# Performance work log

Hardware: AMD Instinct MI355X
Metric: run time of the kernel (lower is better)

Reference implementation:

```python
import jax, jax.numpy as jnp
import numpy as np

SHARPNESS = 2


def setup_inputs() -> dict:
    key = jax.random.key(0)
    k1, k2, k3 = jax.random.split(key, 3)
    x = jax.random.normal(k1, (16, 256, 48, 48), dtype=jnp.float32)
    # 1x1 conv == per-pixel linear: weight (out_c, in_c), bias (out_c,)
    W = jax.random.normal(k2, (256, 256), dtype=jnp.float32) * 0.0625
    bias = jax.random.normal(k3, (256,), dtype=jnp.float32) * 0.01
    return {"x": x, "W": W, "bias": bias}


def reference(x, W, bias):
    b, c, h, w = x.shape
    hw = h * w
    # sample-wide L2 norm over the full (c*h*w) vector (faithful to source)
    xn = jnp.linalg.norm(x.reshape(b, -1), axis=1).reshape(b, 1, 1)
    # NOTE: raw reshapes of the (b,c,h,w)-contiguous tensor, NOT transposes
    x1 = x.reshape(b, hw, c) / xn
    x2 = x.reshape(b, c, hw) / xn
    cos = jnp.einsum('bnc,bcm->bnm', x1, x2)          # (b, hw, hw)
    s = jnp.maximum(cos, 0.0) ** SHARPNESS            # relu^sharpness
    # transform block: 1x1 conv
    tr = jnp.einsum('oc,bchw->bohw', W, x) + bias[None, :, None, None]
    tr = tr.reshape(b, hw, c)                         # raw reshape, as in source
    y = jnp.einsum('bnm,bmc->bnc', s, tr)             # (b, hw, c)
    return y.reshape(b, c, h, w)
```

## Files before the change

kernel.cpp:

```cpp
#include <hip/hip_runtime.h>

#define NB 16
#define NC 256
#define HW 2304
#define CHW 589824

typedef __attribute__((ext_vector_type(8))) short bf16x8;
typedef __attribute__((ext_vector_type(16))) float f32x16;

union BF8 { bf16x8 v; unsigned short u[8]; unsigned d[4]; };

__device__ inline unsigned short f2bf(float f) {
  unsigned u = __builtin_bit_cast(unsigned, f);
  u += 0x7fffu + ((u >> 16) & 1u);
  return (unsigned short)(u >> 16);
}

__device__ inline unsigned f2bf2(float lo, float hi) {
  unsigned r;
  asm("v_cvt_pk_bf16_f32 %0, %1, %2" : "=v"(r) : "v"(lo), "v"(hi));
  return r;
}

__global__ __launch_bounds__(256) void prep_kernel(const float* __restrict__ x,
                                                   const float* __restrict__ W,
                                                   unsigned short* __restrict__ wp,
                                                   unsigned short* __restrict__ x1p,
                                                   unsigned short* __restrict__ xtp,
                                                   double* __restrict__ partials) {
  __shared__ __align__(16) char smem[33344];
  const int bid = blockIdx.x;
  const int tid = threadIdx.x;

  if (bid < 8) {
    const int rt = bid;
    float* tile = (float*)smem;
    const float4* src = (const float4*)(W + (size_t)rt * 32 * 256);
    #pragma unroll
    for (int it = 0; it < 8; ++it) {
      const int i = tid + 256 * it;
      float4 v = src[i];
      const int fi = 4 * i, row = fi >> 8, col = fi & 255;
      *(float4*)&tile[row * 260 + col] = v;
    }
    __syncthreads();
    const int w = tid >> 6, l = tid & 63, l31 = l & 31, h = l >> 5;
    unsigned short* dst = wp + (size_t)rt * 8192;
    #pragma unroll
    for (int ff = 0; ff < 4; ++ff) {
      const int f = 4 * w + ff;
      const float* rp = &tile[l31 * 260 + 16 * f + 8 * h];
      const float4 r0 = *(const float4*)rp;
      const float4 r1 = *(const float4*)(rp + 4);
      BF8 o;
      o.d[0] = f2bf2(r0.x, r0.y);
      o.d[1] = f2bf2(r0.z, r0.w);
      o.d[2] = f2bf2(r1.x, r1.y);
      o.d[3] = f2bf2(r1.z, r1.w);
      *(bf16x8*)(dst + (((size_t)f) * 64 + l) * 8) = o.v;
    }
  } else if (bid < 8 + 1152) {
    const int e = bid - 8;
    const int nb = e % 72, b = e / 72;
    float* tile = (float*)smem;
    double* red = (double*)(smem + 33280);
    const float4* src = (const float4*)(x + (size_t)b * CHW + nb * 8192);
    double ss = 0.0;
    #pragma unroll
    for (int it = 0; it < 8; ++it) {
      const int i = tid + 256 * it;
      float4 v = src[i];
      const int fi = 4 * i, row = fi >> 8, col = fi & 255;
      *(float4*)&tile[row * 260 + col] = v;
      ss += (double)v.x * v.x + (double)v.y * v.y + (double)v.z * v.z + (double)v.w * v.w;
    }
    #pragma unroll
    for (int off = 32; off > 0; off >>= 1) ss += __shfl_down(ss, off, 64);
    const int w = tid >> 6, l = tid & 63;
    if (l == 0) red[w] = ss;
    __syncthreads();
    if (tid == 0) partials[b * 72 + nb] = red[0] + red[1] + red[2] + red[3];
    const int l31 = l & 31, h = l >> 5;
    unsigned short* dst = x1p + (size_t)b * CHW + (size_t)nb * 8192;
    #pragma unroll
    for (int ff = 0; ff < 4; ++ff) {
      const int f = 4 * w + ff;
      const float* rp = &tile[l31 * 260 + 16 * f + 8 * h];
      const float4 r0 = *(const float4*)rp;
      const float4 r1 = *(const float4*)(rp + 4);
      BF8 o;
      o.d[0] = f2bf2(r0.x, r0.y);
      o.d[1] = f2bf2(r0.z, r0.w);
      o.d[2] = f2bf2(r1.x, r1.y);
      o.d[3] = f2bf2(r1.z, r1.w);
      *(bf16x8*)(dst + (((size_t)f) * 64 + l) * 8) = o.v;
    }
  } else {
    const int e = bid - 1160;
    const int mt = e % 36, kt = (e / 36) % 4, b = e / 144;
    const int m0 = mt * 64, k0 = kt * 64;
    float* tile = (float*)smem;
    const float* xb = x + (size_t)b * CHW;
    #pragma unroll
    for (int it = 0; it < 4; ++it) {
      const int i = tid + 256 * it;
      const int row = i >> 4, c4 = (i & 15) * 4;
      float4 v = *(const float4*)(xb + (size_t)(k0 + row) * HW + m0 + c4);
      *(float4*)&tile[row * 68 + c4] = v;
    }
    __syncthreads();
    const int w = tid >> 6, l = tid & 63, l31 = l & 31, h = l >> 5;
    unsigned short* dst = xtp + (size_t)b * CHW;
    #pragma unroll
    for (int pp = 0; pp < 2; ++pp) {
      const int p = 2 * w + pp, mbl = p >> 2, fl = p & 3;
      BF8 o;
      #pragma unroll
      for (int jj = 0; jj < 4; ++jj) {
        const float e0 = tile[(16 * fl + 8 * h + 2 * jj) * 68 + 32 * mbl + l31];
        const float e1 = tile[(16 * fl + 8 * h + 2 * jj + 1) * 68 + 32 * mbl + l31];
        o.d[jj] = f2bf2(e0, e1);
      }
      const int mb = 2 * mt + mbl, f = 4 * kt + fl;
      *(bf16x8*)(dst + (((size_t)mb * 16 + f) * 64 + l) * 8) = o.v;
    }
  }
}

__global__ __launch_bounds__(512, 1) void conv2_kernel(const unsigned short* __restrict__ wp,
                                                       const float* __restrict__ bias,
                                                       const unsigned short* __restrict__ xtp,
                                                       unsigned short* __restrict__ trp,
                                                       const double* __restrict__ partials,
                                                       float* __restrict__ inv_xn2) {
  const int bid = blockIdx.x;
  if (bid == 128) {
    const int t = threadIdx.x;
    if (t >= 256) return;
    const int b = t >> 4, i0 = t & 15;
    double v = 0.0;
    for (int i = i0; i < 72; i += 16) v += partials[b * 72 + i];
    v += __shfl_down(v, 8, 64);
    v += __shfl_down(v, 4, 64);
    v += __shfl_down(v, 2, 64);
    v += __shfl_down(v, 1, 64);
    if (i0 == 0) inv_xn2[b] = (float)(1.0 / v);
    return;
  }
  const int xcd = bid & 7, q = bid >> 3;
  const int b = xcd + 8 * (q & 1);
  const int rt = q >> 1;
  const int tid = threadIdx.x, w = tid >> 6, l = tid & 63, l31 = l & 31, h = l >> 5;
  const unsigned short* xb = xtp + (size_t)b * CHW;

  __shared__ unsigned short tile[32 * 2312];

  bf16x8 af[16];
  #pragma unroll
  for (int f = 0; f < 16; ++f)
    af[f] = *(const bf16x8*)(wp + (((size_t)rt * 16 + f) * 64 + l) * 8);
  float bcol[16];
  #pragma unroll
  for (int reg = 0; reg < 16; ++reg) {
    const int rowl = (reg & 3) + 8 * (reg >> 2) + 4 * h;
    bcol[reg] = bias[32 * rt + rowl];
  }

  for (int i = 0; i < 9; ++i) {
    const int mb = 9 * w + i;
    f32x16 acc;
    #pragma unroll
    for (int r = 0; r < 16; ++r) acc[r] = 0.f;
    #pragma unroll
    for (int f = 0; f < 16; ++f) {
      bf16x8 bv = *(const bf16x8*)(xb + (((size_t)mb * 16 + f) * 64 + l) * 8);
      acc = __builtin_amdgcn_mfma_f32_32x32x16_bf16(af[f], bv, acc, 0, 0, 0);
    }
    #pragma unroll
    for (int p = 0; p < 8; ++p) {
      const int r0 = 2 * p, r1 = 2 * p + 1;
      const int rowl = (r0 & 3) + 8 * (r0 >> 2) + 4 * h;
      const unsigned pk = f2bf2(acc[r0] + bcol[r0], acc[r1] + bcol[r1]);
      tile[rowl * 2312 + mb * 32 + l31] = (unsigned short)pk;
      tile[(rowl + 1) * 2312 + mb * 32 + l31] = (unsigned short)(pk >> 16);
    }
  }
  __syncthreads();

  unsigned short* tb = trp + (size_t)b * CHW;
  for (int si = 0; si < 18; ++si) {
    const int id = 18 * w + si;
    const int kfi = id >> 3, cb8 = id & 7;
    const int mbase = 288 * rt + 16 * kfi;
    const int mb2 = mbase >> 6, kf = (mbase >> 4) & 3;
    BF8 o;
    #pragma unroll
    for (int j = 0; j < 8; ++j) {
      const int m = mbase + 8 * h + j;
      const int a = m / 9, s = m - 9 * a;
      o.u[j] = tile[(a - 32 * rt) * 2312 + 256 * s + 32 * cb8 + l31];
    }
    *(bf16x8*)(tb + (size_t)mb2 * 16384 + (((size_t)cb8 * 4 + kf) * 64 + l) * 8) = o.v;
  }
}

#define CHUNK_BODY(CH, CUR, NXT)                                                                   \
  {                                                                                                \
    const int ch_ = (CH);                                                                          \
    const int pb_ = ch_ & 1;                                                                       \
    f32x16 s0, s1;                                                                                 \
    _Pragma("unroll")                                                                              \
    for (int i = 0; i < 16; ++i) { s0[i] = 0.f; s1[i] = 0.f; }                                     \
    _Pragma("unroll")                                                                              \
    for (int f = 0; f < 16; ++f) {                                                                 \
      bf16x8 a0 = *(const bf16x8*)(Af + f * 512 + lane * 8);                                       \
      bf16x8 a1 = *(const bf16x8*)(Af + (16 + f) * 512 + lane * 8);                                \
      s0 = __builtin_amdgcn_mfma_f32_32x32x16_bf16(a0, CUR[f], s0, 0, 0, 0);                       \
      s1 = __builtin_amdgcn_mfma_f32_32x32x16_bf16(a1, CUR[f], s1, 0, 0, 0);                       \
    }                                                                                              \
    bf16x8 bt0[8], bt1[8];                                                                         \
    _Pragma("unroll")                                                                              \
    for (int kk = 0; kk < 8; ++kk) {                                                               \
      const size_t mb_ = 2 * ch_ + (kk >> 2);                                                      \
      bt0[kk] = *(const bf16x8*)(ttb + mb_ * 16384 + ((size_t)((2 * c) * 4 + (kk & 3))) * 512 + lane * 8);     \
      bt1[kk] = *(const bf16x8*)(ttb + mb_ * 16384 + ((size_t)((2 * c + 1) * 4 + (kk & 3))) * 512 + lane * 8); \
    }                                                                                              \
    _Pragma("unroll")                                                                              \
    for (int reg = 0; reg < 16; ++reg) {                                                           \
      const int rowp = (reg & 3) + 8 * (reg >> 2) + 4 * h;                                         \
      float v0 = fmaxf(s0[reg] * inv2, 0.f); v0 *= v0;                                             \
      float v1 = fmaxf(s1[reg] * inv2, 0.f); v1 *= v1;                                             \
      Pl[pb_][rowp][32 * c + l31] = f2bf(v0);                                                      \
      Pl[pb_][32 + rowp][32 * c + l31] = f2bf(v1);                                                 \
    }                                                                                              \
    const int chn_ = (ch_ < 17) ? ch_ + 1 : 17;                                                    \
    const unsigned short* bpn_ = xtb + (size_t)((4 * chn_ + c) * 16) * 512 + lane * 8;             \
    _Pragma("unroll")                                                                              \
    for (int f = 0; f < 16; ++f) NXT[f] = *(const bf16x8*)(bpn_ + f * 512);                        \
    __syncthreads();                                                                               \
    _Pragma("unroll")                                                                              \
    for (int kk = 0; kk < 8; ++kk) {                                                               \
      bf16x8 pf0 = *(const bf16x8*)&Pl[pb_][l31][16 * kk + 8 * h];                                 \
      bf16x8 pf1 = *(const bf16x8*)&Pl[pb_][32 + l31][16 * kk + 8 * h];                            \
      yacc[0][0] = __builtin_amdgcn_mfma_f32_32x32x16_bf16(pf0, bt0[kk], yacc[0][0], 0, 0, 0);     \
      yacc[1][0] = __builtin_amdgcn_mfma_f32_32x32x16_bf16(pf1, bt0[kk], yacc[1][0], 0, 0, 0);     \
      yacc[0][1] = __builtin_amdgcn_mfma_f32_32x32x16_bf16(pf0, bt1[kk], yacc[0][1], 0, 0, 0);     \
      yacc[1][1] = __builtin_amdgcn_mfma_f32_32x32x16_bf16(pf1, bt1[kk], yacc[1][1], 0, 0, 0);     \
    }                                                                                              \
  }

__global__ __launch_bounds__(256, 2) void fused_kernel(const unsigned short* __restrict__ x1p,
                                                       const unsigned short* __restrict__ xtp,
                                                       const unsigned short* __restrict__ trp,
                                                       const float* __restrict__ inv_xn2,
                                                       float* __restrict__ out) {
  const int bid = blockIdx.x;
  const int xcd = bid & 7, j = bid >> 3;
  const int hi = (j >= 36) ? 1 : 0;
  const int b = xcd + 8 * hi;
  const int nt = j - 36 * hi;
  const unsigned short* x1b = x1p + (size_t)b * CHW + (size_t)nt * 16384;
  const unsigned short* xtb = xtp + (size_t)b * CHW;
  const unsigned short* ttb = trp + (size_t)b * CHW;
  float* ob = out + (size_t)b * CHW;
  const float inv2 = inv_xn2[b];

  const int tid = threadIdx.x;
  const int c = tid >> 6, lane = tid & 63;
  const int l31 = lane & 31, h = lane >> 5;

  __shared__ unsigned short Af[16384];
  __shared__ unsigned short Pl[2][64][136];

  {
    const uint4* gsrc = (const uint4*)x1b;
    uint4* ldst = (uint4*)Af;
    #pragma unroll
    for (int it = 0; it < 8; ++it) ldst[tid + 256 * it] = gsrc[tid + 256 * it];
  }

  bf16x8 bva[16], bvb[16];
  {
    const unsigned short* bp0 = xtb + (size_t)(c * 16) * 512 + lane * 8;
    #pragma unroll
    for (int f = 0; f < 16; ++f) bva[f] = *(const bf16x8*)(bp0 + f * 512);
  }
  __syncthreads();

  f32x16 yacc[2][2];
  #pragma unroll
  for (int nh = 0; nh < 2; ++nh)
    #pragma unroll
    for (int cb = 0; cb < 2; ++cb)
      #pragma unroll
      for (int i = 0; i < 16; ++i) yacc[nh][cb][i] = 0.f;

  for (int ci = 0; ci < 9; ++ci) {
    CHUNK_BODY(2 * ci, bva, bvb)
    CHUNK_BODY(2 * ci + 1, bvb, bva)
  }

  #pragma unroll
  for (int nh = 0; nh < 2; ++nh)
    #pragma unroll
    for (int cb = 0; cb < 2; ++cb) {
      const int col = 64 * c + 32 * cb + l31;
      #pragma unroll
      for (int reg = 0; reg < 16; ++reg) {
        const int rowp = (reg & 3) + 8 * (reg >> 2) + 4 * h;
        ob[(size_t)(64 * nt + 32 * nh + rowp) * NC + col] = yacc[nh][cb][reg];
      }
    }
}

extern "C" void kernel_launch(void* const* d_in, const int* in_sizes, int n_in,
                              void* d_out, int out_size, void* d_ws, size_t ws_size,
                              hipStream_t stream) {
  const float* x    = (const float*)d_in[0];
  const float* W    = (const float*)d_in[1];
  const float* bias = (const float*)d_in[2];
  float* out = (float*)d_out;

  const size_t SZ = (size_t)NB * CHW * sizeof(unsigned short);
  double* partials       = (double*)d_ws;
  float* inv_xn2         = (float*)((char*)d_ws + 16384);
  unsigned short* wp     = (unsigned short*)((char*)d_ws + 32768);
  unsigned short* x1p    = (unsigned short*)((char*)d_ws + 163840);
  unsigned short* xtp    = (unsigned short*)((char*)d_ws + 163840 + SZ);
  unsigned short* trp    = (unsigned short*)((char*)d_ws + 163840 + 3 * SZ);

  prep_kernel<<<3464, 256, 0, stream>>>(x, W, wp, x1p, xtp, partials);
  conv2_kernel<<<129, 512, 0, stream>>>(wp, bias, xtp, trp, partials, inv_xn2);
  fused_kernel<<<576, 256, 0, stream>>>(x1p, xtp, trp, inv_xn2, out);
}
```

Before: 238.0 us.

## Fuse x1 bf16 packing into fused kernel and move norm partials to transpose blocks

Removes the separate prep stage that converted x to a packed bf16 x1 buffer. The fused kernel now reads fp32 x directly and converts it to bf16 fragments while filling shared memory, and the transpose blocks compute the squared-norm partials instead. This saves a full bf16 write plus read of an intermediate tensor and about a third of the prep grid. In exchange, the fused kernel reads fp32 (twice the bytes) with a strided per-lane access pattern and does the conversion work itself.

Measured after the change: 232.8 us. 1.02x faster.

```diff
diff --git a/kernel.cpp b/kernel.cpp
--- a/kernel.cpp
+++ b/kernel.cpp
@@ -25,7 +25,6 @@
 __global__ __launch_bounds__(256) void prep_kernel(const float* __restrict__ x,
                                                    const float* __restrict__ W,
                                                    unsigned short* __restrict__ wp,
-                                                   unsigned short* __restrict__ x1p,
                                                    unsigned short* __restrict__ xtp,
                                                    double* __restrict__ partials) {
   __shared__ __align__(16) char smem[33344];
@@ -59,57 +58,29 @@
       o.d[3] = f2bf2(r1.z, r1.w);
       *(bf16x8*)(dst + (((size_t)f) * 64 + l) * 8) = o.v;
     }
-  } else if (bid < 8 + 1152) {
+  } else {
     const int e = bid - 8;
-    const int nb = e % 72, b = e / 72;
-    float* tile = (float*)smem;
-    double* red = (double*)(smem + 33280);
-    const float4* src = (const float4*)(x + (size_t)b * CHW + nb * 8192);
-    double ss = 0.0;
-    #pragma unroll
-    for (int it = 0; it < 8; ++it) {
-      const int i = tid + 256 * it;
-      float4 v = src[i];
-      const int fi = 4 * i, row = fi >> 8, col = fi & 255;
-      *(float4*)&tile[row * 260 + col] = v;
-      ss += (double)v.x * v.x + (double)v.y * v.y + (double)v.z * v.z + (double)v.w * v.w;
-    }
-    #pragma unroll
-    for (int off = 32; off > 0; off >>= 1) ss += __shfl_down(ss, off, 64);
-    const int w = tid >> 6, l = tid & 63;
-    if (l == 0) red[w] = ss;
-    __syncthreads();
-    if (tid == 0) partials[b * 72 + nb] = red[0] + red[1] + red[2] + red[3];
-    const int l31 = l & 31, h = l >> 5;
-    unsigned short* dst = x1p + (size_t)b * CHW + (size_t)nb * 8192;
-    #pragma unroll
-    for (int ff = 0; ff < 4; ++ff) {
-      const int f = 4 * w + ff;
-      const float* rp = &tile[l31 * 260 + 16 * f + 8 * h];
-      const float4 r0 = *(const float4*)rp;
-      const float4 r1 = *(const float4*)(rp + 4);
-      BF8 o;
-      o.d[0] = f2bf2(r0.x, r0.y);
-      o.d[1] = f2bf2(r0.z, r0.w);
-      o.d[2] = f2bf2(r1.x, r1.y);
-      o.d[3] = f2bf2(r1.z, r1.w);
-      *(bf16x8*)(dst + (((size_t)f) * 64 + l) * 8) = o.v;
-    }
-  } else {
-    const int e = bid - 1160;
     const int mt = e % 36, kt = (e / 36) % 4, b = e / 144;
     const int m0 = mt * 64, k0 = kt * 64;
     float* tile = (float*)smem;
+    double* red = (double*)(smem + 17408);
     const float* xb = x + (size_t)b * CHW;
+    double ss = 0.0;
     #pragma unroll
     for (int it = 0; it < 4; ++it) {
       const int i = tid + 256 * it;
       const int row = i >> 4, c4 = (i & 15) * 4;
       float4 v = *(const float4*)(xb + (size_t)(k0 + row) * HW + m0 + c4);
       *(float4*)&tile[row * 68 + c4] = v;
-    }
+      ss += (double)v.x * v.x + (double)v.y * v.y + (double)v.z * v.z + (double)v.w * v.w;
+    }
+    #pragma unroll
+    for (int off = 32; off > 0; off >>= 1) ss += __shfl_down(ss, off, 64);
+    const int w = tid >> 6, l = tid & 63;
+    if (l == 0) red[w] = ss;
     __syncthreads();
-    const int w = tid >> 6, l = tid & 63, l31 = l & 31, h = l >> 5;
+    if (tid == 0) partials[b * 144 + kt * 36 + mt] = red[0] + red[1] + red[2] + red[3];
+    const int l31 = l & 31, h = l >> 5;
     unsigned short* dst = xtp + (size_t)b * CHW;
     #pragma unroll
     for (int pp = 0; pp < 2; ++pp) {
@@ -139,7 +110,7 @@
     if (t >= 256) return;
     const int b = t >> 4, i0 = t & 15;
     double v = 0.0;
-    for (int i = i0; i < 72; i += 16) v += partials[b * 72 + i];
+    for (int i = i0; i < 144; i += 16) v += partials[b * 144 + i];
     v += __shfl_down(v, 8, 64);
     v += __shfl_down(v, 4, 64);
     v += __shfl_down(v, 2, 64);
@@ -249,7 +220,7 @@
     }                                                                                              \
   }
 
-__global__ __launch_bounds__(256, 2) void fused_kernel(const unsigned short* __restrict__ x1p,
+__global__ __launch_bounds__(256, 2) void fused_kernel(const float* __restrict__ x,
                                                        const unsigned short* __restrict__ xtp,
                                                        const unsigned short* __restrict__ trp,
                                                        const float* __restrict__ inv_xn2,
@@ -259,7 +230,7 @@
   const int hi = (j >= 36) ? 1 : 0;
   const int b = xcd + 8 * hi;
   const int nt = j - 36 * hi;
-  const unsigned short* x1b = x1p + (size_t)b * CHW + (size_t)nt * 16384;
+  const float* xsrc = x + (size_t)b * CHW;
   const unsigned short* xtb = xtp + (size_t)b * CHW;
   const unsigned short* ttb = trp + (size_t)b * CHW;
   float* ob = out + (size_t)b * CHW;
@@ -273,10 +244,21 @@
   __shared__ unsigned short Pl[2][64][136];
 
   {
-    const uint4* gsrc = (const uint4*)x1b;
-    uint4* ldst = (uint4*)Af;
-    #pragma unroll
-    for (int it = 0; it < 8; ++it) ldst[tid + 256 * it] = gsrc[tid + 256 * it];
+    #pragma unroll
+    for (int it = 0; it < 8; ++it) {
+      const int idx = tid + 256 * it;
+      const int f = idx >> 6, l = idx & 63;
+      const int ll31 = l & 31, hh = l >> 5;
+      const float* sp = xsrc + (size_t)(64 * nt + 32 * (f >> 4) + ll31) * 256 + 16 * (f & 15) + 8 * hh;
+      const float4 r0 = *(const float4*)sp;
+      const float4 r1 = *(const float4*)(sp + 4);
+      BF8 o;
+      o.d[0] = f2bf2(r0.x, r0.y);
+      o.d[1] = f2bf2(r0.z, r0.w);
+      o.d[2] = f2bf2(r1.x, r1.y);
+      o.d[3] = f2bf2(r1.z, r1.w);
+      *(bf16x8*)(Af + (size_t)f * 512 + (size_t)l * 8) = o.v;
+    }
   }
 
   bf16x8 bva[16], bvb[16];
@@ -323,13 +305,12 @@
 
   const size_t SZ = (size_t)NB * CHW * sizeof(unsigned short);
   double* partials       = (double*)d_ws;
-  float* inv_xn2         = (float*)((char*)d_ws + 16384);
+  float* inv_xn2         = (float*)((char*)d_ws + 24576);
   unsigned short* wp     = (unsigned short*)((char*)d_ws + 32768);
-  unsigned short* x1p    = (unsigned short*)((char*)d_ws + 163840);
   unsigned short* xtp    = (unsigned short*)((char*)d_ws + 163840 + SZ);
   unsigned short* trp    = (unsigned short*)((char*)d_ws + 163840 + 3 * SZ);
 
-  prep_kernel<<<3464, 256, 0, stream>>>(x, W, wp, x1p, xtp, partials);
+  prep_kernel<<<2312, 256, 0, stream>>>(x, W, wp, xtp, partials);
   conv2_kernel<<<129, 512, 0, stream>>>(wp, bias, xtp, trp, partials, inv_xn2);
-  fused_kernel<<<576, 256, 0, stream>>>(x1p, xtp, trp, inv_xn2, out);
-}
+  fused_kernel<<<576, 256, 0, stream>>>(x, xtp, trp, inv_xn2, out);
+}
```
